# Performance work log

Hardware: AMD Instinct MI355X
Metric: run time of the kernel (lower is better)

Reference implementation:

```python
import jax, jax.numpy as jnp
import numpy as np

D_MODEL = 1024
N_HEADS = 16
HEAD_DIM = D_MODEL // N_HEADS
BATCH = 4
SEQ = 2048
NEG_INF = -1000000000.0  # matches torch masked_fill value in source


def setup_inputs() -> dict:
    key = jax.random.key(0)
    ks = jax.random.split(key, 5)
    scale = 1.0 / np.sqrt(D_MODEL)
    x = jax.random.normal(ks[0], (BATCH, SEQ, D_MODEL), dtype=jnp.float32)
    wq = jax.random.normal(ks[1], (D_MODEL, D_MODEL), dtype=jnp.float32) * scale
    wk = jax.random.normal(ks[2], (D_MODEL, D_MODEL), dtype=jnp.float32) * scale
    wv = jax.random.normal(ks[3], (D_MODEL, D_MODEL), dtype=jnp.float32) * scale
    wo = jax.random.normal(ks[4], (D_MODEL, D_MODEL), dtype=jnp.float32) * scale
    return {"x": x, "wq": wq, "wk": wk, "wv": wv, "wo": wo}


def reference(x, wq, wk, wv, wo):
    b, s, d = x.shape
    # projections (weights applied as x @ W^T, matching nn-style Linear weights)
    q = jnp.einsum('bsd,ed->bse', x, wq).reshape(b, s, N_HEADS, HEAD_DIM).transpose(0, 2, 1, 3)
    k = jnp.einsum('bsd,ed->bse', x, wk).reshape(b, s, N_HEADS, HEAD_DIM).transpose(0, 2, 1, 3)
    v = jnp.einsum('bsd,ed->bse', x, wv).reshape(b, s, N_HEADS, HEAD_DIM).transpose(0, 2, 1, 3)
    # scaled dot-product scores [b, h, s, s]
    scores = jnp.einsum('bhqd,bhkd->bhqk', q, k) / jnp.sqrt(jnp.float32(HEAD_DIM))
    # causal mask: positions strictly above diagonal masked with -1e9
    causal = jnp.triu(jnp.ones((s, s), dtype=bool), k=1)
    scores = jnp.where(causal[None, None], jnp.float32(NEG_INF), scores)
    attn = jax.nn.softmax(scores, axis=-1)
    out = jnp.einsum('bhqk,bhkd->bhqd', attn, v)
    out = out.transpose(0, 2, 1, 3).reshape(b, s, d)
    return jnp.einsum('bsd,ed->bse', out, wo)
```

## Files before the change

### kernel.cpp

```cpp
#include <hip/hip_runtime.h>
#include <hip/hip_bf16.h>

typedef __hip_bfloat16 bf16;
typedef __attribute__((ext_vector_type(8))) short short8;
typedef __attribute__((ext_vector_type(4))) short short4_t;
typedef __attribute__((ext_vector_type(4))) float f32x4;
typedef unsigned int u32;

#define MFMA16(a, b, c) __builtin_amdgcn_mfma_f32_16x16x32_bf16(a, b, c, 0, 0, 0)

static constexpr int S_ = 2048, D_ = 1024, M_ = 8192;
static constexpr size_t SZ = (size_t)M_ * D_;
static constexpr size_t WSZ = (size_t)D_ * D_;
static constexpr float QSCALE = 0.125f * 1.4426950408889634f;

__device__ __forceinline__ void gload16(void* lds, const void* g) {
  __builtin_amdgcn_global_load_lds((const __attribute__((address_space(1))) void*)g,
                                   (__attribute__((address_space(3))) void*)lds, 16, 0, 0);
}

__device__ __forceinline__ short4_t cvt4(const float4 v) {
  short4_t r;
  r[0] = (short)__bfloat16_as_ushort(__float2bfloat16(v.x));
  r[1] = (short)__bfloat16_as_ushort(__float2bfloat16(v.y));
  r[2] = (short)__bfloat16_as_ushort(__float2bfloat16(v.z));
  r[3] = (short)__bfloat16_as_ushort(__float2bfloat16(v.w));
  return r;
}

__device__ __forceinline__ u32 pk2(float a, float b) {
  return (u32)__bfloat16_as_ushort(__float2bfloat16(a)) |
         ((u32)__bfloat16_as_ushort(__float2bfloat16(b)) << 16);
}

__global__ __launch_bounds__(256) void cvt_f32_bf16(const float* __restrict__ in,
                                                    bf16* __restrict__ out, int n4) {
  int stride = gridDim.x * 256;
  for (int i = blockIdx.x * 256 + threadIdx.x; i < n4; i += stride) {
    float4 v = ((const float4*)in)[i];
    *(short4_t*)&out[(size_t)i * 4] = cvt4(v);
  }
}

__global__ __launch_bounds__(256) void cvt_w(const float* __restrict__ s0, const float* __restrict__ s1,
                                             const float* __restrict__ s2, const float* __restrict__ s3,
                                             bf16* __restrict__ dqkv, bf16* __restrict__ dwo, int nseg) {
  const int per = 1 << 18;
  int total = nseg * per;
  for (int i = blockIdx.x * 256 + threadIdx.x; i < total; i += gridDim.x * 256) {
    int seg = i >> 18, off = i & (per - 1);
    const float* s = (seg == 0) ? s0 : (seg == 1) ? s1 : (seg == 2) ? s2 : s3;
    bf16* d = (seg < 3) ? (dqkv + ((size_t)seg << 20)) : dwo;
    float4 v = ((const float4*)s)[off];
    *(short4_t*)&d[(size_t)off * 4] = cvt4(v);
  }
}

__global__ __launch_bounds__(256) void qkv_gemm(const bf16* __restrict__ A,
                                                const bf16* __restrict__ Wqkv,
                                                bf16* __restrict__ QKV) {
  __shared__ __align__(16) bf16 lA[128 * 32];
  __shared__ __align__(16) bf16 lB[128 * 32];
  const int tid = threadIdx.x, lane = tid & 63, w = tid >> 6;
  const int wr = w >> 1, wc = w & 1;
  const int m0 = blockIdx.x * 128;
  const int mat = blockIdx.y >> 3, n0 = (blockIdx.y & 7) * 128;
  const bf16* W = Wqkv + (size_t)mat * WSZ;
  bf16* C = QKV + (size_t)mat * SZ;
  const int l15 = lane & 15, lg = lane >> 4;

  f32x4 zero = {0.f, 0.f, 0.f, 0.f};
  f32x4 acc[4][4];
#pragma unroll
  for (int i = 0; i < 4; i++)
#pragma unroll
    for (int j = 0; j < 4; j++) acc[i][j] = zero;

  for (int kt = 0; kt < 32; ++kt) {
    const int k0 = kt * 32;
#pragma unroll
    for (int i = 0; i < 2; ++i) {
      int c = i * 256 + tid;
      int row = c >> 2, col = (c & 3) * 8;
      gload16(&lA[c * 8], &A[(size_t)(m0 + row) * 1024 + k0 + col]);
      gload16(&lB[c * 8], &W[(size_t)(n0 + row) * 1024 + k0 + col]);
    }
    __syncthreads();

    short8 af[4], bfr[4];
#pragma unroll
    for (int mi = 0; mi < 4; mi++)
      af[mi] = *(const short8*)&lA[(wr * 64 + mi * 16 + l15) * 32 + lg * 8];
#pragma unroll
    for (int ni = 0; ni < 4; ni++)
      bfr[ni] = *(const short8*)&lB[(wc * 64 + ni * 16 + l15) * 32 + lg * 8];
#pragma unroll
    for (int mi = 0; mi < 4; mi++)
#pragma unroll
      for (int ni = 0; ni < 4; ni++) acc[mi][ni] = MFMA16(af[mi], bfr[ni], acc[mi][ni]);
    __syncthreads();
  }

  const float scale = (mat == 0) ? QSCALE : 1.0f;
#pragma unroll
  for (int mi = 0; mi < 4; mi++)
#pragma unroll
    for (int ni = 0; ni < 4; ni++)
#pragma unroll
      for (int r = 0; r < 4; r++) {
        int m = m0 + wr * 64 + mi * 16 + lg * 4 + r;
        int n = n0 + wc * 64 + ni * 16 + l15;
        int b = m >> 11, s = m & 2047, h = n >> 6, dh = n & 63;
        size_t idx = (mat < 2) ? (((size_t)((b << 4) + h) * 2048 + s) * 64 + dh)
                               : (((size_t)((b << 4) + h) * 64 + dh) * 2048 + s);
        C[idx] = __float2bfloat16(acc[mi][ni][r] * scale);
      }
}

__global__ __launch_bounds__(256) void gemm_out(const bf16* __restrict__ A,
                                                const bf16* __restrict__ W,
                                                float* __restrict__ C) {
  __shared__ __align__(16) bf16 lA[128 * 32];
  __shared__ __align__(16) bf16 lB[128 * 32];
  const int tid = threadIdx.x, lane = tid & 63, w = tid >> 6;
  const int wr = w >> 1, wc = w & 1;
  const int m0 = blockIdx.x * 128, n0 = blockIdx.y * 128;
  const int l15 = lane & 15, lg = lane >> 4;

  f32x4 zero = {0.f, 0.f, 0.f, 0.f};
  f32x4 acc[4][4];
#pragma unroll
  for (int i = 0; i < 4; i++)
#pragma unroll
    for (int j = 0; j < 4; j++) acc[i][j] = zero;

  for (int kt = 0; kt < 32; ++kt) {
    const int k0 = kt * 32;
#pragma unroll
    for (int i = 0; i < 2; ++i) {
      int c = i * 256 + tid;
      int row = c >> 2, col = (c & 3) * 8;
      gload16(&lA[c * 8], &A[(size_t)(m0 + row) * 1024 + k0 + col]);
      gload16(&lB[c * 8], &W[(size_t)(n0 + row) * 1024 + k0 + col]);
    }
    __syncthreads();

    short8 af[4], bfr[4];
#pragma unroll
    for (int mi = 0; mi < 4; mi++)
      af[mi] = *(const short8*)&lA[(wr * 64 + mi * 16 + l15) * 32 + lg * 8];
#pragma unroll
    for (int ni = 0; ni < 4; ni++)
      bfr[ni] = *(const short8*)&lB[(wc * 64 + ni * 16 + l15) * 32 + lg * 8];
#pragma unroll
    for (int mi = 0; mi < 4; mi++)
#pragma unroll
      for (int ni = 0; ni < 4; ni++) acc[mi][ni] = MFMA16(af[mi], bfr[ni], acc[mi][ni]);
    __syncthreads();
  }

#pragma unroll
  for (int mi = 0; mi < 4; mi++)
#pragma unroll
    for (int ni = 0; ni < 4; ni++)
#pragma unroll
      for (int r = 0; r < 4; r++) {
        int m = m0 + wr * 64 + mi * 16 + lg * 4 + r;
        int n = n0 + wc * 64 + ni * 16 + l15;
        C[(size_t)m * 1024 + n] = acc[mi][ni][r];
      }
}

__global__ __launch_bounds__(256, 3) void attn_fwd(const bf16* __restrict__ Q,
                                                   const bf16* __restrict__ K,
                                                   const bf16* __restrict__ Vt,
                                                   bf16* __restrict__ O) {
  __shared__ __align__(16) bf16 lK[2][64 * 64];
  __shared__ __align__(16) bf16 lV[2][64 * 64];
  __shared__ __align__(16) bf16 lP[4][32 * 64];
  const int tid = threadIdx.x, lane = tid & 63, w = tid >> 6;
  const int l15 = lane & 15, lg = lane >> 4;
  const int bh = blockIdx.x;
  const int qb = 15 - blockIdx.y;
  const int q0 = qb * 128 + w * 32;
  const bf16* Qb = Q + (size_t)bh * S_ * 64;
  const bf16* Kb = K + (size_t)bh * S_ * 64;
  const bf16* Vb = Vt + (size_t)bh * 64 * S_;
  bf16* Pw = lP[w];

  short8 qf[2][2];
#pragma unroll
  for (int mi = 0; mi < 2; mi++)
#pragma unroll
    for (int kd = 0; kd < 2; kd++)
      qf[mi][kd] = *(const short8*)&Qb[(size_t)(q0 + mi * 16 + l15) * 64 + kd * 32 + lg * 8];

  f32x4 zero = {0.f, 0.f, 0.f, 0.f};
  f32x4 acc[2][4];
  float mr[2], lr[2];
#pragma unroll
  for (int mi = 0; mi < 2; mi++) {
    mr[mi] = -1e9f;
    lr[mi] = 0.f;
#pragma unroll
    for (int ni = 0; ni < 4; ni++) acc[mi][ni] = zero;
  }

  const int nch = (qb + 1) * 2;

#define STAGE(buf, c)                                                                   \
  {                                                                                     \
    _Pragma("unroll") for (int i = 0; i < 2; ++i) {                                     \
      int t2 = i * 256 + tid;                                                           \
      int row = t2 >> 3;                                                                \
      int cb = ((t2 & 7) * 16) ^ ((row & 7) << 4);                                      \
      gload16((char*)lK[buf] + t2 * 16, (const char*)Kb + (size_t)((c) * 64 + row) * 128 + cb); \
      gload16((char*)lV[buf] + t2 * 16, (const char*)Vb + (size_t)row * 4096 + (size_t)(c) * 128 + cb); \
    }                                                                                   \
  }

  STAGE(0, 0);
  int cur = 0;
  for (int c = 0; c < nch; ++c) {
    __builtin_amdgcn_s_barrier();
    if (c + 1 < nch) {
      STAGE(cur ^ 1, c + 1);
      asm volatile("s_waitcnt vmcnt(4)" ::: "memory");
    } else {
      asm volatile("s_waitcnt vmcnt(0)" ::: "memory");
    }
    __builtin_amdgcn_s_barrier();

    if (c * 64 <= q0 + 31) {
      const int c0 = c * 64;
      f32x4 sc[2][4];
#pragma unroll
      for (int mi = 0; mi < 2; mi++)
#pragma unroll
        for (int ch = 0; ch < 4; ch++) sc[mi][ch] = zero;
      const char* Kc = (const char*)lK[cur];
      __builtin_amdgcn_s_setprio(1);
#pragma unroll
      for (int kd = 0; kd < 2; ++kd)
#pragma unroll
        for (int ch = 0; ch < 4; ++ch) {
          short8 kf = *(const short8*)(Kc + (ch * 16 + l15) * 128 + ((kd * 64 + lg * 16) ^ ((l15 & 7) << 4)));
          sc[0][ch] = MFMA16(kf, qf[0][kd], sc[0][ch]);
          sc[1][ch] = MFMA16(kf, qf[1][kd], sc[1][ch]);
        }
      __builtin_amdgcn_s_setprio(0);

      if (c0 + 63 > q0) {
#pragma unroll
        for (int mi = 0; mi < 2; mi++) {
          int q = q0 + mi * 16 + l15;
#pragma unroll
          for (int ch = 0; ch < 4; ch++)
#pragma unroll
            for (int r = 0; r < 4; r++) {
              int kv = c0 + ch * 16 + lg * 4 + r;
              if (kv > q) sc[mi][ch][r] = -1e9f;
            }
        }
      }

#pragma unroll
      for (int mi = 0; mi < 2; mi++) {
        float v0 = fmaxf(fmaxf(sc[mi][0][0], sc[mi][0][1]), fmaxf(sc[mi][0][2], sc[mi][0][3]));
        float v1 = fmaxf(fmaxf(sc[mi][1][0], sc[mi][1][1]), fmaxf(sc[mi][1][2], sc[mi][1][3]));
        float v2 = fmaxf(fmaxf(sc[mi][2][0], sc[mi][2][1]), fmaxf(sc[mi][2][2], sc[mi][2][3]));
        float v3 = fmaxf(fmaxf(sc[mi][3][0], sc[mi][3][1]), fmaxf(sc[mi][3][2], sc[mi][3][3]));
        float vmax = fmaxf(fmaxf(v0, v1), fmaxf(v2, v3));
        vmax = fmaxf(vmax, __shfl_xor(vmax, 16));
        vmax = fmaxf(vmax, __shfl_xor(vmax, 32));
        if (!__all(vmax <= mr[mi] + 8.f)) {
          float mn = fmaxf(mr[mi], vmax);
          float corr = exp2f(mr[mi] - mn);
          mr[mi] = mn;
          lr[mi] *= corr;
#pragma unroll
          for (int r = 0; r < 4; r++) {
            float cr = __shfl(corr, (lane & 48) | (((lane >> 4) << 2) + r));
#pragma unroll
            for (int ni = 0; ni < 4; ni++) acc[mi][ni][r] *= cr;
          }
        }
        float ps = 0.f;
#pragma unroll
        for (int ch = 0; ch < 4; ch++)
#pragma unroll
          for (int r = 0; r < 4; r++) {
            float p = exp2f(sc[mi][ch][r] - mr[mi]);
            sc[mi][ch][r] = p;
            ps += p;
          }
        ps += __shfl_xor(ps, 16);
        ps += __shfl_xor(ps, 32);
        lr[mi] += ps;
        int row = mi * 16 + l15;
        char* Pb = (char*)Pw + row * 128;
        int sw = (row & 7) << 4;
#pragma unroll
        for (int ch = 0; ch < 4; ch++) {
          u32 d0 = pk2(sc[mi][ch][0], sc[mi][ch][1]);
          u32 d1 = pk2(sc[mi][ch][2], sc[mi][ch][3]);
          uint2 dd = {d0, d1};
          *(uint2*)(Pb + ((ch * 32 + lg * 8) ^ sw)) = dd;
        }
      }

      asm volatile("s_waitcnt lgkmcnt(0)" ::: "memory");
      const char* Vc = (const char*)lV[cur];
      __builtin_amdgcn_s_setprio(1);
#pragma unroll
      for (int kd = 0; kd < 2; ++kd) {
        short8 pf[2];
#pragma unroll
        for (int mi = 0; mi < 2; mi++)
          pf[mi] = *(const short8*)((const char*)Pw + (mi * 16 + l15) * 128 +
                                    ((kd * 64 + lg * 16) ^ ((l15 & 7) << 4)));
#pragma unroll
        for (int ni = 0; ni < 4; ++ni) {
          short8 vf = *(const short8*)(Vc + (ni * 16 + l15) * 128 + ((kd * 64 + lg * 16) ^ ((l15 & 7) << 4)));
          acc[0][ni] = MFMA16(pf[0], vf, acc[0][ni]);
          acc[1][ni] = MFMA16(pf[1], vf, acc[1][ni]);
        }
      }
      __builtin_amdgcn_s_setprio(0);
    }
    cur ^= 1;
  }
#undef STAGE

  const int b = bh >> 4, h = bh & 15;
#pragma unroll
  for (int mi = 0; mi < 2; mi++) {
    float lrr[4];
#pragma unroll
    for (int r = 0; r < 4; r++)
      lrr[r] = __shfl(lr[mi], (lane & 48) | (((lane >> 4) << 2) + r));
#pragma unroll
    for (int ni = 0; ni < 4; ni++)
#pragma unroll
      for (int r = 0; r < 4; r++) {
        int q = q0 + mi * 16 + lg * 4 + r;
        size_t idx = ((size_t)(b * 2048 + q)) * 1024 + h * 64 + ni * 16 + l15;
        O[idx] = __float2bfloat16(acc[mi][ni][r] / lrr[r]);
      }
  }
}

extern "C" void kernel_launch(void* const* d_in, const int* in_sizes, int n_in,
                              void* d_out, int out_size, void* d_ws, size_t ws_size,
                              hipStream_t stream) {
  const float* x = (const float*)d_in[0];
  const float* wq = (const float*)d_in[1];
  const float* wk = (const float*)d_in[2];
  const float* wv = (const float*)d_in[3];
  const float* wo = (const float*)d_in[4];
  float* out = (float*)d_out;

  bf16* xb = (bf16*)d_ws;
  bf16* Qw = xb + SZ;
  bf16* AO = xb;
  bf16* wqkv = (bf16*)d_out;

  const bool ws_has_wo = ws_size >= (4 * SZ + WSZ) * sizeof(bf16);
  bf16* wob = ws_has_wo ? (xb + 4 * SZ) : Qw;

  dim3 blk(256);
  hipLaunchKernelGGL(cvt_f32_bf16, dim3(2048), blk, 0, stream, x, xb, (int)(SZ / 4));
  hipLaunchKernelGGL(cvt_w, dim3(1024), blk, 0, stream, wq, wk, wv, wo, wqkv, wob,
                     ws_has_wo ? 4 : 3);
  hipLaunchKernelGGL(qkv_gemm, dim3(64, 24), blk, 0, stream, xb, wqkv, Qw);
  hipLaunchKernelGGL(attn_fwd, dim3(64, 16), blk, 0, stream, Qw, Qw + SZ, Qw + 2 * SZ, AO);
  if (!ws_has_wo)
    hipLaunchKernelGGL(cvt_f32_bf16, dim3(512), blk, 0, stream, wo, wob, (int)(WSZ / 4));
  hipLaunchKernelGGL(gemm_out, dim3(64, 8), blk, 0, stream, AO, wob, out);
}
```

Before: 281.8 us.

## Fuse conversion kernels, transpose V-store via swapped MFMA, use native exp2

Merges the x and weight fp32-to-bf16 conversion launches into one kernel. For the V projection it swaps the MFMA operands, so each lane holds consecutive sequence positions and the transposed V store gets better locality. In the attention softmax it uses the hardware exp2 builtin instead of exp2f and splits the row-sum into four partial accumulators. This trades a little exp precision and adds branches in the QKV GEMM for fewer launches and cheaper softmax and stores.

```diff
diff --git a/kernel.cpp b/kernel.cpp
--- a/kernel.cpp
+++ b/kernel.cpp
@@ -8,6 +8,12 @@
 typedef unsigned int u32;
 
 #define MFMA16(a, b, c) __builtin_amdgcn_mfma_f32_16x16x32_bf16(a, b, c, 0, 0, 0)
+
+#if __has_builtin(__builtin_amdgcn_exp2f)
+#define EXP2(x) __builtin_amdgcn_exp2f(x)
+#else
+#define EXP2(x) __expf((x) * 0.6931471805599453f)
+#endif
 
 static constexpr int S_ = 2048, D_ = 1024, M_ = 8192;
 static constexpr size_t SZ = (size_t)M_ * D_;
@@ -42,15 +48,30 @@
   }
 }
 
-__global__ __launch_bounds__(256) void cvt_w(const float* __restrict__ s0, const float* __restrict__ s1,
-                                             const float* __restrict__ s2, const float* __restrict__ s3,
-                                             bf16* __restrict__ dqkv, bf16* __restrict__ dwo, int nseg) {
+__global__ __launch_bounds__(256) void cvt_all(const float* __restrict__ x,
+                                               const float* __restrict__ wq,
+                                               const float* __restrict__ wk,
+                                               const float* __restrict__ wv,
+                                               const float* __restrict__ wo,
+                                               bf16* __restrict__ xb,
+                                               bf16* __restrict__ wqkv,
+                                               bf16* __restrict__ wob, int nseg) {
+  const int X4 = (int)(SZ / 4);
   const int per = 1 << 18;
-  int total = nseg * per;
+  int total = X4 + nseg * per;
   for (int i = blockIdx.x * 256 + threadIdx.x; i < total; i += gridDim.x * 256) {
-    int seg = i >> 18, off = i & (per - 1);
-    const float* s = (seg == 0) ? s0 : (seg == 1) ? s1 : (seg == 2) ? s2 : s3;
-    bf16* d = (seg < 3) ? (dqkv + ((size_t)seg << 20)) : dwo;
+    const float* s;
+    bf16* d;
+    int off;
+    if (i < X4) {
+      s = x; d = xb; off = i;
+    } else {
+      int j = i - X4;
+      int seg = j >> 18;
+      off = j & (per - 1);
+      s = (seg == 0) ? wq : (seg == 1) ? wk : (seg == 2) ? wv : wo;
+      d = (seg < 3) ? (wqkv + ((size_t)seg << 20)) : wob;
+    }
     float4 v = ((const float4*)s)[off];
     *(short4_t*)&d[(size_t)off * 4] = cvt4(v);
   }
@@ -94,27 +115,48 @@
 #pragma unroll
     for (int ni = 0; ni < 4; ni++)
       bfr[ni] = *(const short8*)&lB[(wc * 64 + ni * 16 + l15) * 32 + lg * 8];
+    if (mat == 2) {
+#pragma unroll
+      for (int mi = 0; mi < 4; mi++)
+#pragma unroll
+        for (int ni = 0; ni < 4; ni++) acc[mi][ni] = MFMA16(bfr[ni], af[mi], acc[mi][ni]);
+    } else {
+#pragma unroll
+      for (int mi = 0; mi < 4; mi++)
+#pragma unroll
+        for (int ni = 0; ni < 4; ni++) acc[mi][ni] = MFMA16(af[mi], bfr[ni], acc[mi][ni]);
+    }
+    __syncthreads();
+  }
+
+  if (mat == 2) {
 #pragma unroll
     for (int mi = 0; mi < 4; mi++)
 #pragma unroll
-      for (int ni = 0; ni < 4; ni++) acc[mi][ni] = MFMA16(af[mi], bfr[ni], acc[mi][ni]);
-    __syncthreads();
-  }
-
-  const float scale = (mat == 0) ? QSCALE : 1.0f;
-#pragma unroll
-  for (int mi = 0; mi < 4; mi++)
-#pragma unroll
-    for (int ni = 0; ni < 4; ni++)
-#pragma unroll
-      for (int r = 0; r < 4; r++) {
-        int m = m0 + wr * 64 + mi * 16 + lg * 4 + r;
-        int n = n0 + wc * 64 + ni * 16 + l15;
-        int b = m >> 11, s = m & 2047, h = n >> 6, dh = n & 63;
-        size_t idx = (mat < 2) ? (((size_t)((b << 4) + h) * 2048 + s) * 64 + dh)
-                               : (((size_t)((b << 4) + h) * 64 + dh) * 2048 + s);
-        C[idx] = __float2bfloat16(acc[mi][ni][r] * scale);
-      }
+      for (int ni = 0; ni < 4; ni++)
+#pragma unroll
+        for (int r = 0; r < 4; r++) {
+          int m = m0 + wr * 64 + mi * 16 + l15;
+          int n = n0 + wc * 64 + ni * 16 + lg * 4 + r;
+          int b = m >> 11, s = m & 2047, h = n >> 6, dh = n & 63;
+          size_t idx = ((size_t)((b << 4) + h) * 64 + dh) * 2048 + s;
+          C[idx] = __float2bfloat16(acc[mi][ni][r]);
+        }
+  } else {
+    const float scale = (mat == 0) ? QSCALE : 1.0f;
+#pragma unroll
+    for (int mi = 0; mi < 4; mi++)
+#pragma unroll
+      for (int ni = 0; ni < 4; ni++)
+#pragma unroll
+        for (int r = 0; r < 4; r++) {
+          int m = m0 + wr * 64 + mi * 16 + lg * 4 + r;
+          int n = n0 + wc * 64 + ni * 16 + l15;
+          int b = m >> 11, s = m & 2047, h = n >> 6, dh = n & 63;
+          size_t idx = ((size_t)((b << 4) + h) * 2048 + s) * 64 + dh;
+          C[idx] = __float2bfloat16(acc[mi][ni][r] * scale);
+        }
+  }
 }
 
 __global__ __launch_bounds__(256) void gemm_out(const bf16* __restrict__ A,
@@ -275,7 +317,7 @@
         vmax = fmaxf(vmax, __shfl_xor(vmax, 32));
         if (!__all(vmax <= mr[mi] + 8.f)) {
           float mn = fmaxf(mr[mi], vmax);
-          float corr = exp2f(mr[mi] - mn);
+          float corr = EXP2(mr[mi] - mn);
           mr[mi] = mn;
           lr[mi] *= corr;
 #pragma unroll
@@ -285,15 +327,17 @@
             for (int ni = 0; ni < 4; ni++) acc[mi][ni][r] *= cr;
           }
         }
-        float ps = 0.f;
-#pragma unroll
-        for (int ch = 0; ch < 4; ch++)
-#pragma unroll
-          for (int r = 0; r < 4; r++) {
-            float p = exp2f(sc[mi][ch][r] - mr[mi]);
-            sc[mi][ch][r] = p;
-            ps += p;
-          }
+        float ps0 = 0.f, ps1 = 0.f, ps2 = 0.f, ps3 = 0.f;
+#pragma unroll
+        for (int ch = 0; ch < 4; ch++) {
+          float p0 = EXP2(sc[mi][ch][0] - mr[mi]);
+          float p1 = EXP2(sc[mi][ch][1] - mr[mi]);
+          float p2 = EXP2(sc[mi][ch][2] - mr[mi]);
+          float p3 = EXP2(sc[mi][ch][3] - mr[mi]);
+          sc[mi][ch][0] = p0; sc[mi][ch][1] = p1; sc[mi][ch][2] = p2; sc[mi][ch][3] = p3;
+          ps0 += p0; ps1 += p1; ps2 += p2; ps3 += p3;
+        }
+        float ps = (ps0 + ps1) + (ps2 + ps3);
         ps += __shfl_xor(ps, 16);
         ps += __shfl_xor(ps, 32);
         lr[mi] += ps;
@@ -369,8 +413,7 @@
   bf16* wob = ws_has_wo ? (xb + 4 * SZ) : Qw;
 
   dim3 blk(256);
-  hipLaunchKernelGGL(cvt_f32_bf16, dim3(2048), blk, 0, stream, x, xb, (int)(SZ / 4));
-  hipLaunchKernelGGL(cvt_w, dim3(1024), blk, 0, stream, wq, wk, wv, wo, wqkv, wob,
+  hipLaunchKernelGGL(cvt_all, dim3(2048), blk, 0, stream, x, wq, wk, wv, wo, xb, wqkv, wob,
                      ws_has_wo ? 4 : 3);
   hipLaunchKernelGGL(qkv_gemm, dim3(64, 24), blk, 0, stream, xb, wqkv, Qw);
   hipLaunchKernelGGL(attn_fwd, dim3(64, 16), blk, 0, stream, Qw, Qw + SZ, Qw + 2 * SZ, AO);
```

Result: faster. 259.7 us (-7.8%).
